# Kernel optimization log

Measured on AMD Instinct MI355X. Metric: run time of the kernel, lower is better.

## Reference

```python
import jax, jax.numpy as jnp
import numpy as np

N, E, F_IN, E_DIM, C, H = 50000, 800000, 128, 16, 64, 4
NEG_SLOPE = 0.2  # PyG GATConv default


def _gat_layer(x, src, dst, ea, W, a_s, a_d, We, a_e, b, heads, concat):
    n = x.shape[0]
    # add self loops; self-loop edge_attr = mean of incoming edge_attr (fill_value='mean')
    loop = jnp.arange(n)
    deg = jax.ops.segment_sum(jnp.ones((src.shape[0],), ea.dtype), dst, num_segments=n)
    loop_ea = jax.ops.segment_sum(ea, dst, num_segments=n) / jnp.maximum(deg, 1.0)[:, None]
    src_f = jnp.concatenate([src, loop])
    dst_f = jnp.concatenate([dst, loop])
    ea_f = jnp.concatenate([ea, loop_ea], axis=0)
    ch = W.shape[1] // heads
    xp = (x @ W).reshape(n, heads, ch)                       # [N,H,C]
    a_src = jnp.einsum('nhc,hc->nh', xp, a_s)                # [N,H]
    a_dst = jnp.einsum('nhc,hc->nh', xp, a_d)
    ep = (ea_f @ We).reshape(-1, heads, ch)                  # [E',H,C]
    a_edge = jnp.einsum('ehc,hc->eh', ep, a_e)
    alpha = a_src[src_f] + a_dst[dst_f] + a_edge             # [E',H]
    alpha = jax.nn.leaky_relu(alpha, NEG_SLOPE)
    # segment softmax over destination neighborhoods
    m = jax.ops.segment_max(alpha, dst_f, num_segments=n)
    ex = jnp.exp(alpha - m[dst_f])
    den = jax.ops.segment_sum(ex, dst_f, num_segments=n)
    alpha = ex / (den[dst_f] + 1e-16)
    out = jax.ops.segment_sum(xp[src_f] * alpha[..., None], dst_f, num_segments=n)  # [N,H,C]
    out = out.reshape(n, heads * ch) if concat else out.mean(axis=1)
    return out + b


def setup_inputs() -> dict:
    key = jax.random.key(0)
    ks = jax.random.split(key, 24)
    s = 0.05
    inp = {
        'x': jax.random.normal(ks[0], (N, F_IN), jnp.float32),
        'edge_index': jax.random.randint(ks[1], (2, E), 0, N, jnp.int64 if jax.config.jax_enable_x64 else jnp.int32),
        'edge_attr': jax.random.normal(ks[2], (E, E_DIM), jnp.float32),
        'W0': jax.random.normal(ks[3], (F_IN, H * C), jnp.float32) * s,
        'a_src0': jax.random.normal(ks[4], (H, C), jnp.float32) * s,
        'a_dst0': jax.random.normal(ks[5], (H, C), jnp.float32) * s,
        'We0': jax.random.normal(ks[6], (E_DIM, H * C), jnp.float32) * s,
        'a_e0': jax.random.normal(ks[7], (H, C), jnp.float32) * s,
        'b0': jnp.zeros((H * C,), jnp.float32),
        'W1': jax.random.normal(ks[8], (H * C, H * C), jnp.float32) * s,
        'a_src1': jax.random.normal(ks[9], (H, C), jnp.float32) * s,
        'a_dst1': jax.random.normal(ks[10], (H, C), jnp.float32) * s,
        'We1': jax.random.normal(ks[11], (E_DIM, H * C), jnp.float32) * s,
        'a_e1': jax.random.normal(ks[12], (H, C), jnp.float32) * s,
        'b1': jnp.zeros((H * C,), jnp.float32),
        'W2': jax.random.normal(ks[13], (H * C, C), jnp.float32) * s,
        'a_src2': jax.random.normal(ks[14], (1, C), jnp.float32) * s,
        'a_dst2': jax.random.normal(ks[15], (1, C), jnp.float32) * s,
        'We2': jax.random.normal(ks[16], (E_DIM, C), jnp.float32) * s,
        'a_e2': jax.random.normal(ks[17], (1, C), jnp.float32) * s,
        'b2': jnp.zeros((C,), jnp.float32),
        'lin_w': jax.random.normal(ks[18], (C, 1), jnp.float32) * s,
        'lin_b': jnp.zeros((1,), jnp.float32),
    }
    return inp


def reference(x, edge_index, edge_attr,
              W0, a_src0, a_dst0, We0, a_e0, b0,
              W1, a_src1, a_dst1, We1, a_e1, b1,
              W2, a_src2, a_dst2, We2, a_e2, b2,
              lin_w, lin_b):
    src, dst = edge_index[0], edge_index[1]
    h = _gat_layer(x, src, dst, edge_attr, W0, a_src0, a_dst0, We0, a_e0, b0, H, True)
    h = jax.nn.relu(h)  # dropout is identity in eval mode
    h = _gat_layer(h, src, dst, edge_attr, W1, a_src1, a_dst1, We1, a_e1, b1, H, True)
    h = jax.nn.relu(h)
    h = _gat_layer(h, src, dst, edge_attr, W2, a_src2, a_dst2, We2, a_e2, b2, 1, True)
    h = jax.nn.relu(h)
    out = h @ lin_w + lin_b
    return jax.nn.sigmoid(out).squeeze()
```

## Files before the change

kernel.cpp:

```cpp
#include <hip/hip_runtime.h>
#include <hip/hip_fp16.h>

using f16x8 = __attribute__((ext_vector_type(8))) _Float16;
using f32x4 = __attribute__((ext_vector_type(4))) float;
using f32x2v = __attribute__((ext_vector_type(2))) float;

static __device__ __forceinline__ float wred_sum(float v) {
#pragma unroll
  for (int o = 32; o > 0; o >>= 1) v += __shfl_xor(v, o);
  return v;
}
static __device__ __forceinline__ float lrelu(float x) { return x > 0.f ? x : 0.2f * x; }

__global__ void count_rank(const int* __restrict__ dst, int* __restrict__ deg,
                           int* __restrict__ rank, int E) {
  int i = blockIdx.x * blockDim.x + threadIdx.x;
  if (i < E) rank[i] = atomicAdd(&deg[dst[i]], 1);
}

__global__ __launch_bounds__(256) void scan_part(const int* __restrict__ deg,
                                                 int* __restrict__ bsum, int n) {
  __shared__ int sd[256];
  int tid = threadIdx.x;
  int i = blockIdx.x * 256 + tid;
  sd[tid] = (i < n) ? deg[i] : 0;
  __syncthreads();
#pragma unroll
  for (int d = 128; d > 0; d >>= 1) {
    if (tid < d) sd[tid] += sd[tid + d];
    __syncthreads();
  }
  if (tid == 0) bsum[blockIdx.x] = sd[0];
}

__global__ __launch_bounds__(256) void scan_final(const int* __restrict__ deg,
                                                  const int* __restrict__ bsum,
                                                  int* __restrict__ row_start, int n, int nb) {
  __shared__ int sd[256];
  __shared__ int sbase;
  int tid = threadIdx.x;
  int b = blockIdx.x;
  int v = (tid < nb && tid < b) ? bsum[tid] : 0;
  sd[tid] = v;
  __syncthreads();
#pragma unroll
  for (int d = 128; d > 0; d >>= 1) {
    if (tid < d) sd[tid] += sd[tid + d];
    __syncthreads();
  }
  if (tid == 0) sbase = sd[0];
  __syncthreads();
  int i = b * 256 + tid;
  int dv = (i < n) ? deg[i] : 0;
  sd[tid] = dv;
  __syncthreads();
#pragma unroll
  for (int d = 1; d < 256; d <<= 1) {
    int t = (tid >= d) ? sd[tid - d] : 0;
    __syncthreads();
    sd[tid] += t;
    __syncthreads();
  }
  int incl = sd[tid];
  if (i < n) row_start[i] = sbase + incl - dv;
  if (i == n - 1) row_start[n] = sbase + incl;
}

__global__ void scatter_edges(const int* __restrict__ src, const int* __restrict__ dst,
                              const int* __restrict__ row_start, const int* __restrict__ rank,
                              int2* __restrict__ se, int E) {
  int i = blockIdx.x * blockDim.x + threadIdx.x;
  if (i < E) {
    int d = dst[i];
    int pos = row_start[d] + rank[i];
    se[pos] = make_int2(src[i], i);
  }
}

__global__ __launch_bounds__(256) void prep_weights(
    const float* __restrict__ W0, __half* __restrict__ W0t,
    const float* __restrict__ W1, __half* __restrict__ W1t,
    const float* __restrict__ W2, __half* __restrict__ W2t,
    const float* __restrict__ We0, const float* __restrict__ ae0w,
    const float* __restrict__ We1, const float* __restrict__ ae1w,
    const float* __restrict__ We2, const float* __restrict__ ae2w,
    float* __restrict__ wv) {
  int b = blockIdx.x;
  if (b >= 448) {
    int t = threadIdx.x;
    if (t < 144) {
      int k = t >> 4, d = t & 15;
      const float* We; const float* aev; int h; int HC;
      if (k < 4)      { We = We0; aev = ae0w; h = k;     HC = 256; }
      else if (k < 8) { We = We1; aev = ae1w; h = k - 4; HC = 256; }
      else            { We = We2; aev = ae2w; h = 0;     HC = 64; }
      float sum = 0.f;
#pragma unroll
      for (int c = 0; c < 64; ++c) sum += We[(size_t)d * HC + h * 64 + c] * aev[h * 64 + c];
      wv[k * 16 + d] = sum;
    }
    return;
  }
  const float* W; __half* Wt; int K, Nc, bx, by;
  if (b < 128)      { W = W0; Wt = W0t; K = 128; Nc = 256; bx = b & 15; by = b >> 4; }
  else if (b < 384) { int c = b - 128; W = W1; Wt = W1t; K = 256; Nc = 256; bx = c & 15; by = c >> 4; }
  else              { int c = b - 384; W = W2; Wt = W2t; K = 256; Nc = 64;  bx = c & 3;  by = c >> 2; }
  int n = bx * 16 + (threadIdx.x & 15);
  int k = by * 16 + (threadIdx.x >> 4);
  if (n < Nc && k < K) Wt[(size_t)n * K + k] = __float2half(W[(size_t)k * Nc + n]);
}

__global__ __launch_bounds__(256) void edge_ae(const float* __restrict__ ea,
                                               const int2* __restrict__ se,
                                               const float* __restrict__ wv,
                                               float* __restrict__ ae0, float* __restrict__ ae1,
                                               float* __restrict__ ae2, int E) {
  __shared__ float swv[144];
  if (threadIdx.x < 144) swv[threadIdx.x] = wv[threadIdx.x];
  __syncthreads();
  int p = blockIdx.x * blockDim.x + threadIdx.x;
  if (p >= E) return;
  int e = se[p].y;
  const float4* er = (const float4*)(ea + (size_t)e * 16);
  float4 v0 = er[0], v1 = er[1], v2 = er[2], v3 = er[3];
  float ev[16] = {v0.x, v0.y, v0.z, v0.w, v1.x, v1.y, v1.z, v1.w,
                  v2.x, v2.y, v2.z, v2.w, v3.x, v3.y, v3.z, v3.w};
  float r[9];
#pragma unroll
  for (int k = 0; k < 9; ++k) {
    float s = 0.f;
#pragma unroll
    for (int d = 0; d < 16; ++d) s += ev[d] * swv[k * 16 + d];
    r[k] = s;
  }
  *(float4*)(ae0 + (size_t)p * 4) = make_float4(r[0], r[1], r[2], r[3]);
  *(float4*)(ae1 + (size_t)p * 4) = make_float4(r[4], r[5], r[6], r[7]);
  ae2[p] = r[8];
}

template <int BN, bool AF32, int HS, bool XF8>
__global__ __launch_bounds__(256) void gemm_f16mfma(const void* __restrict__ Av,
                                                    const __half* __restrict__ Bt,
                                                    void* __restrict__ Cv,
                                                    const float* __restrict__ as_w,
                                                    const float* __restrict__ ad_w,
                                                    float* __restrict__ asb,
                                                    float* __restrict__ adb,
                                                    int M, int K, int Nc) {
  constexpr int BM = 128, BK = 64;
  constexpr int LDT = BK + 8;
  constexpr int WN = BN / 2;
  constexpr int NFN = WN / 16;
  __shared__ __half As[BM][LDT];
  __shared__ __half Bs[BN][LDT];
  const int tid = threadIdx.x;
  const int lane = tid & 63, wave = tid >> 6;
  const int wr = wave >> 1, wc = wave & 1;
  const int bm = blockIdx.x * BM;
  const int bn = blockIdx.y * BN;
  const int r15 = lane & 15, kgrp = lane >> 4;
  f32x4 acc[4][NFN] = {};
  for (int k0 = 0; k0 < K; k0 += BK) {
    if constexpr (AF32) {
      const float* A = (const float*)Av;
#pragma unroll
      for (int i = 0; i < 8; ++i) {
        int chunk = tid + i * 256;
        int row = chunk >> 4, kc = (chunk & 15) * 4;
        int grow = bm + row;
        float4 v = make_float4(0, 0, 0, 0);
        if (grow < M) v = *(const float4*)(A + (size_t)grow * K + k0 + kc);
        __half2 h01 = __floats2half2_rn(v.x, v.y);
        __half2 h23 = __floats2half2_rn(v.z, v.w);
        uint2 u;
        u.x = *(unsigned*)&h01;
        u.y = *(unsigned*)&h23;
        *(uint2*)&As[row][kc] = u;
      }
    } else {
      const __half* A = (const __half*)Av;
#pragma unroll
      for (int i = 0; i < 4; ++i) {
        int chunk = tid + i * 256;
        int row = chunk >> 3, kc = (chunk & 7) * 8;
        int grow = bm + row;
        float4 v = make_float4(0, 0, 0, 0);
        if (grow < M) v = *(const float4*)(A + (size_t)grow * K + k0 + kc);
        *(float4*)&As[row][kc] = v;
      }
    }
#pragma unroll
    for (int i = 0; i < BN / 32; ++i) {
      int chunk = tid + i * 256;
      int row = chunk >> 3, kc = (chunk & 7) * 8;
      *(float4*)&Bs[row][kc] = *(const float4*)(Bt + (size_t)(bn + row) * K + k0 + kc);
    }
    __syncthreads();
#pragma unroll
    for (int kk = 0; kk < BK; kk += 32) {
      f16x8 af[4], bf[NFN];
#pragma unroll
      for (int mi = 0; mi < 4; ++mi)
        af[mi] = *(const f16x8*)&As[wr * 64 + mi * 16 + r15][kk + kgrp * 8];
#pragma unroll
      for (int ni = 0; ni < NFN; ++ni)
        bf[ni] = *(const f16x8*)&Bs[wc * WN + ni * 16 + r15][kk + kgrp * 8];
#pragma unroll
      for (int mi = 0; mi < 4; ++mi)
#pragma unroll
        for (int ni = 0; ni < NFN; ++ni)
          acc[mi][ni] = __builtin_amdgcn_mfma_f32_16x16x32_f16(af[mi], bf[ni], acc[mi][ni], 0, 0, 0);
    }
    __syncthreads();
  }
  float asw[NFN], adw[NFN];
#pragma unroll
  for (int ni = 0; ni < NFN; ++ni) {
    int gcol = bn + wc * WN + ni * 16 + r15;
    asw[ni] = as_w[gcol];
    adw[ni] = ad_w[gcol];
  }
  const int hidx = (bn + wc * WN) >> 6;
#pragma unroll
  for (int mi = 0; mi < 4; ++mi) {
#pragma unroll
    for (int r = 0; r < 4; ++r) {
      int grow = bm + wr * 64 + mi * 16 + kgrp * 4 + r;
      bool valid = grow < M;
      float sdot = 0.f, ddot = 0.f;
#pragma unroll
      for (int ni = 0; ni < NFN; ++ni) {
        float v = acc[mi][ni][r];
        if (valid) {
          int gcol = bn + wc * WN + ni * 16 + r15;
          if constexpr (XF8) {
            unsigned pk = (unsigned)__builtin_amdgcn_cvt_pk_fp8_f32(v, v, 0, false);
            ((unsigned char*)Cv)[(size_t)grow * Nc + gcol] = (unsigned char)(pk & 0xff);
          } else {
            ((__half*)Cv)[(size_t)grow * Nc + gcol] = __float2half(v);
          }
        }
        sdot = fmaf(v, asw[ni], sdot);
        ddot = fmaf(v, adw[ni], ddot);
      }
#pragma unroll
      for (int o = 8; o >= 1; o >>= 1) {
        sdot += __shfl_xor(sdot, o);
        ddot += __shfl_xor(ddot, o);
      }
      if (valid && r15 == 0) {
        if constexpr (HS == 1) {
          atomicAdd(&asb[grow], sdot);
          atomicAdd(&adb[grow], ddot);
        } else {
          asb[(size_t)grow * HS + hidx] = sdot;
          adb[(size_t)grow * HS + hidx] = ddot;
        }
      }
    }
  }
}

__global__ __launch_bounds__(256) void agg_heads4(
    const unsigned char* __restrict__ xp, const int2* __restrict__ se,
    const int* __restrict__ row_start, const float* __restrict__ asb,
    const float* __restrict__ adb, const float* __restrict__ ae,
    const float* __restrict__ bias, __half* __restrict__ out, int N) {
  __shared__ float sw[4][256];
  __shared__ int ssrc[4][64];
  int wave = threadIdx.x >> 6, lane = threadIdx.x & 63;
  int n = blockIdx.x * 4 + wave;
  if (n >= N) return;
  int beg = row_start[n], end = row_start[n + 1];
  int deg = end - beg;
  int hsel = lane >> 4;
  float4 adn = *(const float4*)(adb + (size_t)n * 4);
  float4 asn = *(const float4*)(asb + (size_t)n * 4);
  float invd = 1.f / fmaxf((float)deg, 1.f);
  float acc0 = 0, acc1 = 0, acc2 = 0, acc3 = 0;
  float den0 = 0, den1 = 0, den2 = 0, den3 = 0;
  float al0, al1, al2, al3, exl0, exl1, exl2, exl3;
  const int loff = lane << 2;

  if (deg <= 64) {
    int j = beg + lane;
    bool act = j < end;
    int s = 0;
    float4 asv = make_float4(0, 0, 0, 0), aev = make_float4(0, 0, 0, 0);
    if (act) {
      s = se[j].x;
      asv = *(const float4*)(asb + (size_t)s * 4);
      aev = *(const float4*)(ae + (size_t)j * 4);
    }
    float ex0 = act ? __expf(lrelu(asv.x + adn.x + aev.x)) : 0.f;
    float ex1 = act ? __expf(lrelu(asv.y + adn.y + aev.y)) : 0.f;
    float ex2 = act ? __expf(lrelu(asv.z + adn.z + aev.z)) : 0.f;
    float ex3 = act ? __expf(lrelu(asv.w + adn.w + aev.w)) : 0.f;
    float aes0 = wred_sum(aev.x), aes1 = wred_sum(aev.y), aes2 = wred_sum(aev.z), aes3 = wred_sum(aev.w);
    al0 = lrelu(asn.x + adn.x + aes0 * invd);
    al1 = lrelu(asn.y + adn.y + aes1 * invd);
    al2 = lrelu(asn.z + adn.z + aes2 * invd);
    al3 = lrelu(asn.w + adn.w + aes3 * invd);
    exl0 = __expf(al0); exl1 = __expf(al1); exl2 = __expf(al2); exl3 = __expf(al3);
    den0 = wred_sum(ex0); den1 = wred_sum(ex1); den2 = wred_sum(ex2); den3 = wred_sum(ex3);
    *(float4*)&sw[wave][lane << 2] = make_float4(ex0, ex1, ex2, ex3);
    ssrc[wave][lane] = s << 8;
    asm volatile("" ::: "memory");
    int cnt = deg;
    int sj0 = ssrc[wave][0], sj1 = ssrc[wave][1], sj2 = ssrc[wave][2], sj3 = ssrc[wave][3];
    unsigned B0 = *(const unsigned*)(xp + sj0 + loff);
    unsigned B1 = *(const unsigned*)(xp + sj1 + loff);
    unsigned B2 = *(const unsigned*)(xp + sj2 + loff);
    unsigned B3 = *(const unsigned*)(xp + sj3 + loff);
    for (int t = 0; t < cnt; t += 4) {
      {
        float w = sw[wave][((t + 0) << 2) + hsel];
        f32x2v lo = __builtin_amdgcn_cvt_pk_f32_fp8((int)B0, false);
        f32x2v hi = __builtin_amdgcn_cvt_pk_f32_fp8((int)B0, true);
        acc0 = fmaf(w, lo[0], acc0); acc1 = fmaf(w, lo[1], acc1);
        acc2 = fmaf(w, hi[0], acc2); acc3 = fmaf(w, hi[1], acc3);
        int ns = ssrc[wave][(t + 4) & 63];
        B0 = *(const unsigned*)(xp + ns + loff);
      }
      {
        float w = sw[wave][((t + 1) << 2) + hsel];
        f32x2v lo = __builtin_amdgcn_cvt_pk_f32_fp8((int)B1, false);
        f32x2v hi = __builtin_amdgcn_cvt_pk_f32_fp8((int)B1, true);
        acc0 = fmaf(w, lo[0], acc0); acc1 = fmaf(w, lo[1], acc1);
        acc2 = fmaf(w, hi[0], acc2); acc3 = fmaf(w, hi[1], acc3);
        int ns = ssrc[wave][(t + 5) & 63];
        B1 = *(const unsigned*)(xp + ns + loff);
      }
      {
        float w = sw[wave][((t + 2) << 2) + hsel];
        f32x2v lo = __builtin_amdgcn_cvt_pk_f32_fp8((int)B2, false);
        f32x2v hi = __builtin_amdgcn_cvt_pk_f32_fp8((int)B2, true);
        acc0 = fmaf(w, lo[0], acc0); acc1 = fmaf(w, lo[1], acc1);
        acc2 = fmaf(w, hi[0], acc2); acc3 = fmaf(w, hi[1], acc3);
        int ns = ssrc[wave][(t + 6) & 63];
        B2 = *(const unsigned*)(xp + ns + loff);
      }
      {
        float w = sw[wave][((t + 3) << 2) + hsel];
        f32x2v lo = __builtin_amdgcn_cvt_pk_f32_fp8((int)B3, false);
        f32x2v hi = __builtin_amdgcn_cvt_pk_f32_fp8((int)B3, true);
        acc0 = fmaf(w, lo[0], acc0); acc1 = fmaf(w, lo[1], acc1);
        acc2 = fmaf(w, hi[0], acc2); acc3 = fmaf(w, hi[1], acc3);
        int ns = ssrc[wave][(t + 7) & 63];
        B3 = *(const unsigned*)(xp + ns + loff);
      }
    }
  } else {
    float aes0 = 0, aes1 = 0, aes2 = 0, aes3 = 0;
    for (int base = beg; base < end; base += 64) {
      int j = base + lane;
      if (j < end) {
        float4 aev = *(const float4*)(ae + (size_t)j * 4);
        aes0 += aev.x; aes1 += aev.y; aes2 += aev.z; aes3 += aev.w;
      }
    }
    aes0 = wred_sum(aes0); aes1 = wred_sum(aes1); aes2 = wred_sum(aes2); aes3 = wred_sum(aes3);
    al0 = lrelu(asn.x + adn.x + aes0 * invd);
    al1 = lrelu(asn.y + adn.y + aes1 * invd);
    al2 = lrelu(asn.z + adn.z + aes2 * invd);
    al3 = lrelu(asn.w + adn.w + aes3 * invd);
    exl0 = __expf(al0); exl1 = __expf(al1); exl2 = __expf(al2); exl3 = __expf(al3);
    for (int base = beg; base < end; base += 64) {
      int j = base + lane;
      float ex0 = 0, ex1 = 0, ex2 = 0, ex3 = 0;
      int s = 0;
      if (j < end) {
        s = se[j].x;
        float4 asv = *(const float4*)(asb + (size_t)s * 4);
        float4 aev = *(const float4*)(ae + (size_t)j * 4);
        ex0 = __expf(lrelu(asv.x + adn.x + aev.x));
        ex1 = __expf(lrelu(asv.y + adn.y + aev.y));
        ex2 = __expf(lrelu(asv.z + adn.z + aev.z));
        ex3 = __expf(lrelu(asv.w + adn.w + aev.w));
        den0 += ex0; den1 += ex1; den2 += ex2; den3 += ex3;
      }
      int cnt = min(64, end - base);
      for (int t = 0; t < cnt; ++t) {
        int sj = __shfl(s, t);
        float w0 = __shfl(ex0, t), w1 = __shfl(ex1, t), w2 = __shfl(ex2, t), w3 = __shfl(ex3, t);
        float w = hsel == 0 ? w0 : (hsel == 1 ? w1 : (hsel == 2 ? w2 : w3));
        unsigned u = *(const unsigned*)(xp + ((size_t)sj << 8) + loff);
        f32x2v lo = __builtin_amdgcn_cvt_pk_f32_fp8((int)u, false);
        f32x2v hi = __builtin_amdgcn_cvt_pk_f32_fp8((int)u, true);
        acc0 = fmaf(w, lo[0], acc0);
        acc1 = fmaf(w, lo[1], acc1);
        acc2 = fmaf(w, hi[0], acc2);
        acc3 = fmaf(w, hi[1], acc3);
      }
    }
    den0 = wred_sum(den0); den1 = wred_sum(den1); den2 = wred_sum(den2); den3 = wred_sum(den3);
  }

  den0 += exl0; den1 += exl1; den2 += exl2; den3 += exl3;
  float exh = hsel == 0 ? exl0 : (hsel == 1 ? exl1 : (hsel == 2 ? exl2 : exl3));
  {
    unsigned u = *(const unsigned*)(xp + ((size_t)n << 8) + loff);
    f32x2v lo = __builtin_amdgcn_cvt_pk_f32_fp8((int)u, false);
    f32x2v hi = __builtin_amdgcn_cvt_pk_f32_fp8((int)u, true);
    acc0 = fmaf(exh, lo[0], acc0);
    acc1 = fmaf(exh, lo[1], acc1);
    acc2 = fmaf(exh, hi[0], acc2);
    acc3 = fmaf(exh, hi[1], acc3);
  }
  float denh = hsel == 0 ? den0 : (hsel == 1 ? den1 : (hsel == 2 ? den2 : den3));
  float rden = 1.f / (denh + 1e-16f);
  float4 bv = *(const float4*)(bias + (lane << 2));
  __half2 o01 = __floats2half2_rn(fmaxf(acc0 * rden + bv.x, 0.f), fmaxf(acc1 * rden + bv.y, 0.f));
  __half2 o23 = __floats2half2_rn(fmaxf(acc2 * rden + bv.z, 0.f), fmaxf(acc3 * rden + bv.w, 0.f));
  uint2 u;
  u.x = *(unsigned*)&o01;
  u.y = *(unsigned*)&o23;
  *(uint2*)(out + (size_t)n * 256 + (lane << 2)) = u;
}

__global__ __launch_bounds__(256) void agg1_final(
    const __half* __restrict__ xp, const int2* __restrict__ se,
    const int* __restrict__ row_start, const float* __restrict__ asb,
    const float* __restrict__ adb, const float* __restrict__ ae,
    const float* __restrict__ b2, const float* __restrict__ lin_w,
    const float* __restrict__ lin_b, float* __restrict__ out, int N) {
  __shared__ float sw1[4][64];
  __shared__ int ssrc1[4][64];
  int wave = threadIdx.x >> 6, lane = threadIdx.x & 63;
  int n = blockIdx.x * 4 + wave;
  if (n >= N) return;
  int beg = row_start[n], end = row_start[n + 1];
  int deg = end - beg;
  float adn = adb[n], asn = asb[n];
  float invd = 1.f / fmaxf((float)deg, 1.f);
  float al, exl, acc = 0, den = 0;

  if (deg <= 64) {
    int j = beg + lane;
    bool act = j < end;
    int s = 0;
    float aev = 0, asvs = 0;
    if (act) { s = se[j].x; aev = ae[j]; asvs = asb[s]; }
    float ex = act ? __expf(lrelu(asvs + adn + aev)) : 0.f;
    float aes = wred_sum(aev);
    al = lrelu(asn + adn + aes * invd);
    exl = __expf(al);
    den = wred_sum(ex);
    sw1[wave][lane] = ex;
    ssrc1[wave][lane] = s;
    asm volatile("" ::: "memory");
    int cnt = deg;
    int sj0 = ssrc1[wave][0], sj1 = ssrc1[wave][1], sj2 = ssrc1[wave][2], sj3 = ssrc1[wave][3];
    __half H0 = xp[((size_t)sj0 << 6) + lane];
    __half H1 = xp[((size_t)sj1 << 6) + lane];
    __half H2 = xp[((size_t)sj2 << 6) + lane];
    __half H3 = xp[((size_t)sj3 << 6) + lane];
    for (int t = 0; t < cnt; t += 4) {
      {
        float w = sw1[wave][t + 0];
        acc = fmaf(w, __half2float(H0), acc);
        int ns = ssrc1[wave][(t + 4) & 63];
        H0 = xp[((size_t)ns << 6) + lane];
      }
      {
        float w = sw1[wave][t + 1];
        acc = fmaf(w, __half2float(H1), acc);
        int ns = ssrc1[wave][(t + 5) & 63];
        H1 = xp[((size_t)ns << 6) + lane];
      }
      {
        float w = sw1[wave][t + 2];
        acc = fmaf(w, __half2float(H2), acc);
        int ns = ssrc1[wave][(t + 6) & 63];
        H2 = xp[((size_t)ns << 6) + lane];
      }
      {
        float w = sw1[wave][t + 3];
        acc = fmaf(w, __half2float(H3), acc);
        int ns = ssrc1[wave][(t + 7) & 63];
        H3 = xp[((size_t)ns << 6) + lane];
      }
    }
  } else {
    float aes = 0;
    for (int base = beg; base < end; base += 64) {
      int j = base + lane;
      if (j < end) aes += ae[j];
    }
    aes = wred_sum(aes);
    al = lrelu(asn + adn + aes * invd);
    exl = __expf(al);
    for (int base = beg; base < end; base += 64) {
      int j = base + lane;
      float ex = 0;
      int s = 0;
      if (j < end) {
        s = se[j].x;
        ex = __expf(lrelu(asb[s] + adn + ae[j]));
        den += ex;
      }
      int cnt = min(64, end - base);
      for (int t = 0; t < cnt; ++t) {
        int sj = __shfl(s, t);
        float w = __shfl(ex, t);
        acc = fmaf(w, __half2float(xp[((size_t)sj << 6) + lane]), acc);
      }
    }
    den = wred_sum(den);
  }

  den += exl;
  acc = fmaf(exl, __half2float(xp[((size_t)n << 6) + lane]), acc);
  float h = fmaxf(acc / (den + 1e-16f) + b2[lane], 0.f);
  float p = wred_sum(h * lin_w[lane]);
  if (lane == 0) out[n] = 1.f / (1.f + __expf(-(p + lin_b[0])));
}

extern "C" void kernel_launch(void* const* d_in, const int* in_sizes, int n_in,
                              void* d_out, int out_size, void* d_ws, size_t ws_size,
                              hipStream_t stream) {
  const float* x    = (const float*)d_in[0];
  const int*   ei   = (const int*)d_in[1];
  const float* ea   = (const float*)d_in[2];
  const float* W0   = (const float*)d_in[3];
  const float* as0w = (const float*)d_in[4];
  const float* ad0w = (const float*)d_in[5];
  const float* We0  = (const float*)d_in[6];
  const float* ae0w = (const float*)d_in[7];
  const float* b0   = (const float*)d_in[8];
  const float* W1   = (const float*)d_in[9];
  const float* as1w = (const float*)d_in[10];
  const float* ad1w = (const float*)d_in[11];
  const float* We1  = (const float*)d_in[12];
  const float* ae1w = (const float*)d_in[13];
  const float* b1   = (const float*)d_in[14];
  const float* W2   = (const float*)d_in[15];
  const float* as2w = (const float*)d_in[16];
  const float* ad2w = (const float*)d_in[17];
  const float* We2  = (const float*)d_in[18];
  const float* ae2w = (const float*)d_in[19];
  const float* b2   = (const float*)d_in[20];
  const float* linw = (const float*)d_in[21];
  const float* linb = (const float*)d_in[22];

  const int N = in_sizes[0] / 128;
  const int E = in_sizes[1] / 2;
  const int* src = ei;
  const int* dst = ei + E;

  char* p = (char*)d_ws;
  auto alloc = [&](size_t bytes) {
    char* r = p;
    p += (bytes + 255) & ~size_t(255);
    return r;
  };
  __half*        bufAh = (__half*)alloc((size_t)N * 256 * 2);
  unsigned char* xp8   = (unsigned char*)alloc((size_t)N * 256);
  __half*        xph2  = (__half*)alloc((size_t)N * 64 * 2);
  __half*        W0t   = (__half*)alloc((size_t)256 * 128 * 2);
  __half*        W1t   = (__half*)alloc((size_t)256 * 256 * 2);
  __half*        W2t   = (__half*)alloc((size_t)64 * 256 * 2);
  float*         asb0  = (float*)alloc((size_t)N * 4 * 4);
  float*         adb0  = (float*)alloc((size_t)N * 4 * 4);
  float*         asb1  = (float*)alloc((size_t)N * 4 * 4);
  float*         adb1  = (float*)alloc((size_t)N * 4 * 4);
  char*   zbase      = p;
  int*    deg        = (int*)alloc((size_t)N * 4);
  float*  asb2       = (float*)alloc((size_t)N * 4);
  float*  adb2       = (float*)alloc((size_t)N * 4);
  size_t  zspan      = (size_t)(p - zbase);
  int*    rank       = (int*)alloc((size_t)E * 4);
  int2*   se         = (int2*)alloc((size_t)E * 8);
  float*  ae0s       = (float*)alloc((size_t)E * 4 * 4);
  float*  ae1s       = (float*)alloc((size_t)E * 4 * 4);
  float*  ae2s       = (float*)alloc((size_t)E * 4);
  int*    row_start  = (int*)alloc((size_t)(N + 1) * 4);
  int*    bsum       = (int*)alloc((size_t)256 * 4);
  float*  wv         = (float*)alloc(144 * 4);

  int nb = (N + 255) / 256;
  int eb = (E + 255) / 256;
  hipMemsetAsync(zbase, 0, zspan, stream);
  count_rank<<<eb, 256, 0, stream>>>(dst, deg, rank, E);
  scan_part<<<nb, 256, 0, stream>>>(deg, bsum, N);
  scan_final<<<nb, 256, 0, stream>>>(deg, bsum, row_start, N, nb);
  scatter_edges<<<eb, 256, 0, stream>>>(src, dst, row_start, rank, se, E);
  prep_weights<<<449, 256, 0, stream>>>(W0, W0t, W1, W1t, W2, W2t,
                                        We0, ae0w, We1, ae1w, We2, ae2w, wv);
  edge_ae<<<eb, 256, 0, stream>>>(ea, se, wv, ae0s, ae1s, ae2s, E);

  int gm = (N + 127) / 128;
  int nwb = (N + 3) / 4;
  gemm_f16mfma<128, true, 4, true><<<dim3(gm, 2), 256, 0, stream>>>(
      x, W0t, xp8, as0w, ad0w, asb0, adb0, N, 128, 256);
  agg_heads4<<<nwb, 256, 0, stream>>>(xp8, se, row_start, asb0, adb0, ae0s, b0, bufAh, N);
  gemm_f16mfma<128, false, 4, true><<<dim3(gm, 2), 256, 0, stream>>>(
      bufAh, W1t, xp8, as1w, ad1w, asb1, adb1, N, 256, 256);
  agg_heads4<<<nwb, 256, 0, stream>>>(xp8, se, row_start, asb1, adb1, ae1s, b1, bufAh, N);
  gemm_f16mfma<64, false, 1, false><<<dim3(gm, 1), 256, 0, stream>>>(
      bufAh, W2t, xph2, as2w, ad2w, asb2, adb2, N, 256, 64);
  agg1_final<<<nwb, 256, 0, stream>>>(xph2, se, row_start, asb2, adb2, ae2s, b2, linw, linb,
                                      (float*)d_out, N);
}
```

Before: 281.6 us.

## Double-buffer LDS tiles in fp16 MFMA GEMM with register prefetch

```diff
diff --git a/kernel.cpp b/kernel.cpp
--- a/kernel.cpp
+++ b/kernel.cpp
@@ -147,12 +147,12 @@
                                                     float* __restrict__ asb,
                                                     float* __restrict__ adb,
                                                     int M, int K, int Nc) {
-  constexpr int BM = 128, BK = 64;
+  constexpr int BM = 128, BK = 32;
   constexpr int LDT = BK + 8;
   constexpr int WN = BN / 2;
   constexpr int NFN = WN / 16;
-  __shared__ __half As[BM][LDT];
-  __shared__ __half Bs[BN][LDT];
+  __shared__ __half As[2][BM][LDT];
+  __shared__ __half Bs[2][BN][LDT];
   const int tid = threadIdx.x;
   const int lane = tid & 63, wave = tid >> 6;
   const int wr = wave >> 1, wc = wave & 1;
@@ -160,59 +160,102 @@
   const int bn = blockIdx.y * BN;
   const int r15 = lane & 15, kgrp = lane >> 4;
   f32x4 acc[4][NFN] = {};
-  for (int k0 = 0; k0 < K; k0 += BK) {
+  float4 ar32_0, ar32_1, ar32_2, ar32_3;
+  float4 ar16_0, ar16_1;
+  float4 br_0, br_1;
+
+  auto issue_loads = [&](int t) {
+    int k0 = t * BK;
     if constexpr (AF32) {
       const float* A = (const float*)Av;
 #pragma unroll
-      for (int i = 0; i < 8; ++i) {
+      for (int i = 0; i < 4; ++i) {
         int chunk = tid + i * 256;
-        int row = chunk >> 4, kc = (chunk & 15) * 4;
+        int row = chunk >> 3, kc = (chunk & 7) * 4;
         int grow = bm + row;
         float4 v = make_float4(0, 0, 0, 0);
         if (grow < M) v = *(const float4*)(A + (size_t)grow * K + k0 + kc);
+        if (i == 0) ar32_0 = v; else if (i == 1) ar32_1 = v;
+        else if (i == 2) ar32_2 = v; else ar32_3 = v;
+      }
+    } else {
+      const __half* A = (const __half*)Av;
+#pragma unroll
+      for (int i = 0; i < 2; ++i) {
+        int chunk = tid + i * 256;
+        int row = chunk >> 2, kc = (chunk & 3) * 8;
+        int grow = bm + row;
+        float4 v = make_float4(0, 0, 0, 0);
+        if (grow < M) v = *(const float4*)(A + (size_t)grow * K + k0 + kc);
+        if (i == 0) ar16_0 = v; else ar16_1 = v;
+      }
+    }
+#pragma unroll
+    for (int i = 0; i < BN / 64; ++i) {
+      int chunk = tid + i * 256;
+      int row = chunk >> 2, kc = (chunk & 3) * 8;
+      float4 v = *(const float4*)(Bt + (size_t)(bn + row) * K + t * BK + kc);
+      if (i == 0) br_0 = v; else br_1 = v;
+    }
+  };
+  auto write_lds = [&](int buf) {
+    if constexpr (AF32) {
+#pragma unroll
+      for (int i = 0; i < 4; ++i) {
+        int chunk = tid + i * 256;
+        int row = chunk >> 3, kc = (chunk & 7) * 4;
+        float4 v = (i == 0) ? ar32_0 : (i == 1) ? ar32_1 : (i == 2) ? ar32_2 : ar32_3;
         __half2 h01 = __floats2half2_rn(v.x, v.y);
         __half2 h23 = __floats2half2_rn(v.z, v.w);
         uint2 u;
         u.x = *(unsigned*)&h01;
         u.y = *(unsigned*)&h23;
-        *(uint2*)&As[row][kc] = u;
+        *(uint2*)&As[buf][row][kc] = u;
       }
     } else {
-      const __half* A = (const __half*)Av;
-#pragma unroll
-      for (int i = 0; i < 4; ++i) {
+#pragma unroll
+      for (int i = 0; i < 2; ++i) {
         int chunk = tid + i * 256;
-        int row = chunk >> 3, kc = (chunk & 7) * 8;
-        int grow = bm + row;
-        float4 v = make_float4(0, 0, 0, 0);
-        if (grow < M) v = *(const float4*)(A + (size_t)grow * K + k0 + kc);
-        *(float4*)&As[row][kc] = v;
-      }
-    }
-#pragma unroll
-    for (int i = 0; i < BN / 32; ++i) {
+        int row = chunk >> 2, kc = (chunk & 3) * 8;
+        *(float4*)&As[buf][row][kc] = (i == 0) ? ar16_0 : ar16_1;
+      }
+    }
+#pragma unroll
+    for (int i = 0; i < BN / 64; ++i) {
       int chunk = tid + i * 256;
-      int row = chunk >> 3, kc = (chunk & 7) * 8;
-      *(float4*)&Bs[row][kc] = *(const float4*)(Bt + (size_t)(bn + row) * K + k0 + kc);
-    }
-    __syncthreads();
-#pragma unroll
-    for (int kk = 0; kk < BK; kk += 32) {
-      f16x8 af[4], bf[NFN];
-#pragma unroll
-      for (int mi = 0; mi < 4; ++mi)
-        af[mi] = *(const f16x8*)&As[wr * 64 + mi * 16 + r15][kk + kgrp * 8];
+      int row = chunk >> 2, kc = (chunk & 3) * 8;
+      *(float4*)&Bs[buf][row][kc] = (i == 0) ? br_0 : br_1;
+    }
+  };
+  auto compute = [&](int buf) {
+    f16x8 af[4], bf[NFN];
+#pragma unroll
+    for (int mi = 0; mi < 4; ++mi)
+      af[mi] = *(const f16x8*)&As[buf][wr * 64 + mi * 16 + r15][kgrp * 8];
+#pragma unroll
+    for (int ni = 0; ni < NFN; ++ni)
+      bf[ni] = *(const f16x8*)&Bs[buf][wc * WN + ni * 16 + r15][kgrp * 8];
+#pragma unroll
+    for (int mi = 0; mi < 4; ++mi)
 #pragma unroll
       for (int ni = 0; ni < NFN; ++ni)
-        bf[ni] = *(const f16x8*)&Bs[wc * WN + ni * 16 + r15][kk + kgrp * 8];
-#pragma unroll
-      for (int mi = 0; mi < 4; ++mi)
-#pragma unroll
-        for (int ni = 0; ni < NFN; ++ni)
-          acc[mi][ni] = __builtin_amdgcn_mfma_f32_16x16x32_f16(af[mi], bf[ni], acc[mi][ni], 0, 0, 0);
-    }
-    __syncthreads();
-  }
+        acc[mi][ni] = __builtin_amdgcn_mfma_f32_16x16x32_f16(af[mi], bf[ni], acc[mi][ni], 0, 0, 0);
+  };
+
+  const int nt = K / BK;
+  issue_loads(0);
+  write_lds(0);
+  __syncthreads();
+  for (int t = 0; t < nt; ++t) {
+    int cur = t & 1;
+    if (t + 1 < nt) issue_loads(t + 1);
+    compute(cur);
+    if (t + 1 < nt) {
+      write_lds(cur ^ 1);
+      __syncthreads();
+    }
+  }
+
   float asw[NFN], adw[NFN];
 #pragma unroll
   for (int ni = 0; ni < NFN; ++ni) {
```

New measurement: 272.7 us, median of 2. -3.2%, faster.
